# Optimization experiments

Hardware: AMD Instinct MI355X
Metric: run time of the kernel (lower is better)

The kernel has to match this reference:

```python
import jax, jax.numpy as jnp
import numpy as np

D_MODEL = 2048
DT_RANK = 64


def setup_inputs() -> dict:
    key = jax.random.key(0)
    ks = jax.random.split(key, 9)
    x = jax.random.normal(ks[0], (4, 2048, D_MODEL), dtype=jnp.float32)
    A = jax.random.normal(ks[1], (D_MODEL, D_MODEL), dtype=jnp.float32)
    B = jax.random.normal(ks[2], (D_MODEL, D_MODEL), dtype=jnp.float32)
    C = jax.random.normal(ks[3], (D_MODEL, D_MODEL), dtype=jnp.float32)
    Dp = jax.random.normal(ks[4], (1, D_MODEL), dtype=jnp.float32)
    # dt_project: Linear(d_model -> dt_rank); dt_project_out: Linear(dt_rank -> d_model)
    lim1 = 1.0 / np.sqrt(D_MODEL)
    W1 = jax.random.uniform(ks[5], (DT_RANK, D_MODEL), minval=-lim1, maxval=lim1, dtype=jnp.float32)
    b1 = jax.random.uniform(ks[6], (DT_RANK,), minval=-lim1, maxval=lim1, dtype=jnp.float32)
    lim2 = 1.0 / np.sqrt(DT_RANK)
    W2 = jax.random.uniform(ks[7], (D_MODEL, DT_RANK), minval=-lim2, maxval=lim2, dtype=jnp.float32)
    b2 = jax.random.uniform(ks[8], (D_MODEL,), minval=-lim2, maxval=lim2, dtype=jnp.float32)
    return {"x": x, "A": A, "B": B, "C": C, "Dp": Dp, "W1": W1, "b1": b1, "W2": W2, "b2": b2}


def reference(x, A, B, C, Dp, W1, b1, W2, b2):
    # dt = Linear_out(gelu(Linear_in(x)))  -- torch uses exact (erf) gelu
    h = jax.nn.gelu(jnp.einsum('bld,rd->blr', x, W1) + b1, approximate=False)
    dt = jnp.einsum('blr,dr->bld', h, W2) + b2
    # per-timestep loop collapses to one batched GEMM: x @ (A+B+C)
    out = jnp.einsum('bld,ds->bls', x, A + B + C)
    return out * dt + Dp  # Dp broadcasts (1, d_model)
```

## Files before the change

kernel.cpp:

```cpp
#include <hip/hip_runtime.h>
#include <stdint.h>

#define D 2048
#define R 64
#define M_TOTAL 8192

typedef float f32x4 __attribute__((ext_vector_type(4)));
typedef __bf16 bf16x8 __attribute__((ext_vector_type(8)));
typedef unsigned short u16x8 __attribute__((ext_vector_type(8)));
typedef unsigned short u16x4 __attribute__((ext_vector_type(4)));

__device__ __forceinline__ unsigned short f2bf(float f) {
  unsigned u = __builtin_bit_cast(unsigned, f);
  u += 0x7FFFu + ((u >> 16) & 1u);
  return (unsigned short)(u >> 16);
}

__device__ __forceinline__ void gload_lds16(const void* g, void* l) {
  __builtin_amdgcn_global_load_lds(
      (const __attribute__((address_space(1))) void*)g,
      (__attribute__((address_space(3))) void*)l, 16, 0, 0);
}

__global__ __launch_bounds__(256) void prep_kernel(
    const float* __restrict__ x, const float* __restrict__ A,
    const float* __restrict__ B, const float* __restrict__ C,
    const float* __restrict__ w1, const float* __restrict__ b1,
    const float* __restrict__ w2,
    unsigned short* __restrict__ xbf, unsigned short* __restrict__ st,
    unsigned short* __restrict__ w2bf, unsigned short* __restrict__ hbf) {
  __shared__ unsigned short plds[10240];
  int t = threadIdx.x;
  int bx = blockIdx.x;
  if (bx < 128) {
    int m0 = bx * 64;
    int row = t >> 2, c8 = (t & 3) * 8;
    const float* xp = x + (size_t)(m0 + row) * D + c8;
    const float* wp = w1 + (size_t)row * D + c8;
    unsigned short* xop = xbf + (size_t)(m0 + row) * D + c8;
    unsigned short* sX = plds;
    unsigned short* sW = plds + 5120;
    int w = t >> 6, lm = t & 15, lk = (t & 63) >> 4;
    f32x4 acc[4] = {};
    float4 rx0 = *(const float4*)(xp);
    float4 rx1 = *(const float4*)(xp + 4);
    float4 rw0 = *(const float4*)(wp);
    float4 rw1 = *(const float4*)(wp + 4);
#pragma unroll 1
    for (int kt = 0; kt < 64; ++kt) {
      int buf = (kt & 1) * 2560;
      u16x8 ox = { f2bf(rx0.x), f2bf(rx0.y), f2bf(rx0.z), f2bf(rx0.w),
                   f2bf(rx1.x), f2bf(rx1.y), f2bf(rx1.z), f2bf(rx1.w) };
      u16x8 ow = { f2bf(rw0.x), f2bf(rw0.y), f2bf(rw0.z), f2bf(rw0.w),
                   f2bf(rw1.x), f2bf(rw1.y), f2bf(rw1.z), f2bf(rw1.w) };
      *(u16x8*)(sX + buf + row * 40 + c8) = ox;
      *(u16x8*)(sW + buf + row * 40 + c8) = ow;
      *(u16x8*)(xop + kt * 32) = ox;
      __syncthreads();
      if (kt < 63) {
        rx0 = *(const float4*)(xp + (kt + 1) * 32);
        rx1 = *(const float4*)(xp + (kt + 1) * 32 + 4);
        rw0 = *(const float4*)(wp + (kt + 1) * 32);
        rw1 = *(const float4*)(wp + (kt + 1) * 32 + 4);
      }
      bf16x8 a = __builtin_bit_cast(bf16x8, *(const u16x8*)(sX + buf + (w * 16 + lm) * 40 + lk * 8));
#pragma unroll
      for (int j = 0; j < 4; ++j) {
        bf16x8 b = __builtin_bit_cast(bf16x8, *(const u16x8*)(sW + buf + (j * 16 + lm) * 40 + lk * 8));
        acc[j] = __builtin_amdgcn_mfma_f32_16x16x32_bf16(a, b, acc[j], 0, 0, 0);
      }
    }
    int m_base = m0 + w * 16 + lk * 4;
#pragma unroll
    for (int j = 0; j < 4; ++j) {
      int n = j * 16 + lm;
      float bv = b1[n];
#pragma unroll
      for (int r = 0; r < 4; ++r) {
        float v = acc[j][r] + bv;
        float g = 0.5f * v * (1.0f + erff(v * 0.70710678118654752f));
        hbf[(size_t)(m_base + r) * R + n] = f2bf(g);
      }
    }
  } else if (bx < 1152) {
    unsigned short (*lds)[68] = (unsigned short(*)[68])plds;
    int id = bx - 128;
    int tk = id >> 5, tn = id & 31;
    int k0 = tk * 64, n0 = tn * 64;
#pragma unroll
    for (int q = 0; q < 4; ++q) {
      int row = q * 16 + (t >> 4);
      int col = (t & 15) * 4;
      size_t off = (size_t)(k0 + row) * D + n0 + col;
      float4 a = *(const float4*)(A + off);
      float4 b = *(const float4*)(B + off);
      float4 c = *(const float4*)(C + off);
      u16x4 o = { f2bf(a.x + b.x + c.x), f2bf(a.y + b.y + c.y),
                  f2bf(a.z + b.z + c.z), f2bf(a.w + b.w + c.w) };
      *(u16x4*)(&lds[row][col]) = o;
    }
    __syncthreads();
    int n = t >> 2, kc = (t & 3) * 16;
    u16x8 v0, v1;
#pragma unroll
    for (int jj = 0; jj < 8; ++jj) v0[jj] = lds[kc + jj][n];
#pragma unroll
    for (int jj = 0; jj < 8; ++jj) v1[jj] = lds[kc + 8 + jj][n];
    size_t ooff = (size_t)(n0 + n) * D + k0 + kc;
    *(u16x8*)(st + ooff) = v0;
    *(u16x8*)(st + ooff + 8) = v1;
  } else {
    const int NW4 = (D * R) / 4;
    for (int i = (bx - 1152) * 256 + t; i < NW4; i += 8 * 256) {
      float4 v = ((const float4*)w2)[i];
      u16x4 o = { f2bf(v.x), f2bf(v.y), f2bf(v.z), f2bf(v.w) };
      *(u16x4*)(w2bf + (size_t)i * 4) = o;
    }
  }
}

__global__ __launch_bounds__(512, 2) void gemm_kernel(
    const unsigned short* __restrict__ xbf, const unsigned short* __restrict__ st,
    const unsigned short* __restrict__ hbf, const unsigned short* __restrict__ w2bf,
    const float* __restrict__ b2, const float* __restrict__ dp,
    float* __restrict__ out) {
  __shared__ unsigned short sA[2 * 16384];
  __shared__ unsigned short sB[2 * 16384];
  const int tid = threadIdx.x;
  const int w = tid >> 6, l = tid & 63, lk = l >> 4, lm = l & 15;
  const int wm = w >> 2, wn = w & 3;
  int bid = blockIdx.x;
  int wg = (bid & 7) * 32 + (bid >> 3);
  int mb = wg >> 3, nb = wg & 7;
  int m0 = mb * 256, n0 = nb * 256;

  const int kg = (tid & 7) ^ ((tid >> 3) & 7);
  const unsigned short* gA = xbf + (size_t)(m0 + (tid >> 3)) * D + kg * 8;
  const unsigned short* gB = st + (size_t)(n0 + (tid >> 3)) * D + kg * 8;
  const int dstw = w * 512;

  const int s7 = lm & 7;
  const int gsw0 = (lk ^ s7) * 8;
  const int gsw1 = ((4 | lk) ^ s7) * 8;
  const int arow = (wm * 128 + lm) * 64;
  const int brow = (wn * 64 + lm) * 64;

  f32x4 acc[8][4] = {};

#define STAGE(gptr, sbuf, T, h) do { \
    const unsigned short* g_ = (gptr) + (size_t)((h) * 128) * D + (T) * 64; \
    unsigned short* d_ = (sbuf) + (((T) & 1) * 16384 + (h) * 8192 + dstw); \
    gload_lds16(g_, d_); \
    gload_lds16(g_ + 64 * D, d_ + 4096); } while (0)

#define LD8(buf, off) __builtin_bit_cast(bf16x8, *(const u16x8*)((buf) + (off)))

  STAGE(gA, sA, 0, 0); STAGE(gA, sA, 0, 1);
  STAGE(gB, sB, 0, 0); STAGE(gB, sB, 0, 1);
  asm volatile("s_waitcnt vmcnt(0)" ::: "memory");
  __builtin_amdgcn_s_barrier();

  const int NT = D / 64;
#pragma unroll 1
  for (int kt = 0; kt < NT; ++kt) {
    const unsigned short* bufA = sA + (kt & 1) * 16384;
    const unsigned short* bufB = sB + (kt & 1) * 16384;
    bf16x8 a[4][2], b0[2][2], b1[2][2];

    #pragma unroll
    for (int i = 0; i < 4; ++i) {
      a[i][0] = LD8(bufA, arow + i * 1024 + gsw0);
      a[i][1] = LD8(bufA, arow + i * 1024 + gsw1);
    }
    #pragma unroll
    for (int j = 0; j < 2; ++j) {
      b0[j][0] = LD8(bufB, brow + j * 1024 + gsw0);
      b0[j][1] = LD8(bufB, brow + j * 1024 + gsw1);
    }
    if (kt + 1 < NT) { STAGE(gA, sA, kt + 1, 0); STAGE(gA, sA, kt + 1, 1); }
    __builtin_amdgcn_s_barrier();
    asm volatile("s_waitcnt lgkmcnt(0)" ::: "memory");
    __builtin_amdgcn_s_setprio(1);
    #pragma unroll
    for (int i = 0; i < 4; ++i)
      #pragma unroll
      for (int j = 0; j < 2; ++j) {
        acc[i][j] = __builtin_amdgcn_mfma_f32_16x16x32_bf16(a[i][0], b0[j][0], acc[i][j], 0, 0, 0);
        acc[i][j] = __builtin_amdgcn_mfma_f32_16x16x32_bf16(a[i][1], b0[j][1], acc[i][j], 0, 0, 0);
      }
    __builtin_amdgcn_s_setprio(0);
    __builtin_amdgcn_s_barrier();

    #pragma unroll
    for (int j = 0; j < 2; ++j) {
      b1[j][0] = LD8(bufB, brow + (j + 2) * 1024 + gsw0);
      b1[j][1] = LD8(bufB, brow + (j + 2) * 1024 + gsw1);
    }
    if (kt + 1 < NT) STAGE(gB, sB, kt + 1, 0);
    __builtin_amdgcn_s_barrier();
    asm volatile("s_waitcnt lgkmcnt(0)" ::: "memory");
    __builtin_amdgcn_s_setprio(1);
    #pragma unroll
    for (int i = 0; i < 4; ++i)
      #pragma unroll
      for (int j = 0; j < 2; ++j) {
        acc[i][j + 2] = __builtin_amdgcn_mfma_f32_16x16x32_bf16(a[i][0], b1[j][0], acc[i][j + 2], 0, 0, 0);
        acc[i][j + 2] = __builtin_amdgcn_mfma_f32_16x16x32_bf16(a[i][1], b1[j][1], acc[i][j + 2], 0, 0, 0);
      }
    __builtin_amdgcn_s_setprio(0);
    __builtin_amdgcn_s_barrier();

    #pragma unroll
    for (int i = 0; i < 4; ++i) {
      a[i][0] = LD8(bufA, arow + (i + 4) * 1024 + gsw0);
      a[i][1] = LD8(bufA, arow + (i + 4) * 1024 + gsw1);
    }
    if (kt + 1 < NT) STAGE(gB, sB, kt + 1, 1);
    __builtin_amdgcn_s_barrier();
    asm volatile("s_waitcnt lgkmcnt(0)" ::: "memory");
    __builtin_amdgcn_s_setprio(1);
    #pragma unroll
    for (int i = 0; i < 4; ++i)
      #pragma unroll
      for (int j = 0; j < 2; ++j) {
        acc[i + 4][j + 2] = __builtin_amdgcn_mfma_f32_16x16x32_bf16(a[i][0], b1[j][0], acc[i + 4][j + 2], 0, 0, 0);
        acc[i + 4][j + 2] = __builtin_amdgcn_mfma_f32_16x16x32_bf16(a[i][1], b1[j][1], acc[i + 4][j + 2], 0, 0, 0);
      }
    __builtin_amdgcn_s_setprio(0);
    __builtin_amdgcn_s_barrier();

    __builtin_amdgcn_s_setprio(1);
    #pragma unroll
    for (int i = 0; i < 4; ++i)
      #pragma unroll
      for (int j = 0; j < 2; ++j) {
        acc[i + 4][j] = __builtin_amdgcn_mfma_f32_16x16x32_bf16(a[i][0], b0[j][0], acc[i + 4][j], 0, 0, 0);
        acc[i + 4][j] = __builtin_amdgcn_mfma_f32_16x16x32_bf16(a[i][1], b0[j][1], acc[i + 4][j], 0, 0, 0);
      }
    __builtin_amdgcn_s_setprio(0);
    asm volatile("s_waitcnt vmcnt(0)" ::: "memory");
    __builtin_amdgcn_s_barrier();
  }

  bf16x8 wb0[4], wb1[4];
  float b2v[4], dpv[4];
#pragma unroll
  for (int j = 0; j < 4; ++j) {
    int n = n0 + wn * 64 + j * 16 + lm;
    const u16x8* wp = (const u16x8*)(w2bf + (size_t)n * R + lk * 8);
    wb0[j] = __builtin_bit_cast(bf16x8, wp[0]);
    wb1[j] = __builtin_bit_cast(bf16x8, wp[4]);
    b2v[j] = b2[n];
    dpv[j] = dp[n];
  }
#pragma unroll
  for (int mi = 0; mi < 8; ++mi) {
    int hrow = m0 + wm * 128 + mi * 16 + lm;
    const u16x8* hp = (const u16x8*)(hbf + (size_t)hrow * R + lk * 8);
    bf16x8 ha0 = __builtin_bit_cast(bf16x8, hp[0]);
    bf16x8 ha1 = __builtin_bit_cast(bf16x8, hp[4]);
    int mbase = m0 + wm * 128 + mi * 16 + lk * 4;
#pragma unroll
    for (int j = 0; j < 4; ++j) {
      f32x4 dt = {};
      dt = __builtin_amdgcn_mfma_f32_16x16x32_bf16(ha0, wb0[j], dt, 0, 0, 0);
      dt = __builtin_amdgcn_mfma_f32_16x16x32_bf16(ha1, wb1[j], dt, 0, 0, 0);
      int n = n0 + wn * 64 + j * 16 + lm;
#pragma unroll
      for (int r = 0; r < 4; ++r) {
        float val = acc[mi][j][r] * (dt[r] + b2v[j]) + dpv[j];
        out[(size_t)(mbase + r) * D + n] = val;
      }
    }
  }
#undef STAGE
#undef LD8
}

extern "C" void kernel_launch(void* const* d_in, const int* in_sizes, int n_in,
                              void* d_out, int out_size, void* d_ws, size_t ws_size,
                              hipStream_t stream) {
  const float* x  = (const float*)d_in[0];
  const float* A  = (const float*)d_in[1];
  const float* B  = (const float*)d_in[2];
  const float* C  = (const float*)d_in[3];
  const float* Dp = (const float*)d_in[4];
  const float* W1 = (const float*)d_in[5];
  const float* b1 = (const float*)d_in[6];
  const float* W2 = (const float*)d_in[7];
  const float* b2 = (const float*)d_in[8];
  float* out = (float*)d_out;

  uint8_t* ws = (uint8_t*)d_ws;
  unsigned short* xbf  = (unsigned short*)ws;
  unsigned short* st   = (unsigned short*)(ws + (32u << 20));
  unsigned short* w2bf = (unsigned short*)(ws + (40u << 20));
  unsigned short* hbf  = (unsigned short*)(ws + (41u << 20));

  prep_kernel<<<1160, 256, 0, stream>>>(x, A, B, C, W1, b1, W2, xbf, st, w2bf, hbf);
  gemm_kernel<<<256, 512, 0, stream>>>(xbf, st, hbf, w2bf, b2, Dp, out);
}
```

Measured before the change: 119.0 us.

## Split prep kernel K dimension across 512-thread blocks with swizzled LDS and deeper prefetch

```diff
diff --git a/kernel.cpp b/kernel.cpp
--- a/kernel.cpp
+++ b/kernel.cpp
@@ -22,85 +22,110 @@
       (__attribute__((address_space(3))) void*)l, 16, 0, 0);
 }
 
-__global__ __launch_bounds__(256) void prep_kernel(
+__global__ __launch_bounds__(512) void prep_kernel(
     const float* __restrict__ x, const float* __restrict__ A,
     const float* __restrict__ B, const float* __restrict__ C,
     const float* __restrict__ w1, const float* __restrict__ b1,
     const float* __restrict__ w2,
     unsigned short* __restrict__ xbf, unsigned short* __restrict__ st,
     unsigned short* __restrict__ w2bf, unsigned short* __restrict__ hbf) {
-  __shared__ unsigned short plds[10240];
-  int t = threadIdx.x;
-  int bx = blockIdx.x;
+  __shared__ unsigned short plds[16384];
+  const int t = threadIdx.x;
+  const int bx = blockIdx.x;
+
   if (bx < 128) {
-    int m0 = bx * 64;
-    int row = t >> 2, c8 = (t & 3) * 8;
-    const float* xp = x + (size_t)(m0 + row) * D + c8;
-    const float* wp = w1 + (size_t)row * D + c8;
-    unsigned short* xop = xbf + (size_t)(m0 + row) * D + c8;
     unsigned short* sX = plds;
-    unsigned short* sW = plds + 5120;
-    int w = t >> 6, lm = t & 15, lk = (t & 63) >> 4;
+    unsigned short* sW = plds + 8192;
+    const int m0 = bx * 64;
+    const int kh = t >> 8;
+    const int row = (t & 255) >> 2;
+    const int c = t & 3;
+    const float* xp = x + (size_t)(m0 + row) * D + kh * 1024 + c * 8;
+    const float* wp = w1 + (size_t)row * D + kh * 1024 + c * 8;
+    unsigned short* xop = xbf + (size_t)(m0 + row) * D + kh * 1024 + c * 8;
+    const int wslot = (c ^ ((row >> 1) & 3)) * 8;
+    unsigned short* sXw = sX + kh * 4096 + row * 32 + wslot;
+    unsigned short* sWw = sW + kh * 4096 + row * 32 + wslot;
+    const int w = t >> 6, l = t & 63, lm = l & 15, lk = l >> 4;
+    const int khw = w >> 2, wg = w & 3;
+    const int rslot = (lk ^ ((lm >> 1) & 3)) * 8;
+    const unsigned short* sXr = sX + khw * 4096 + (wg * 16 + lm) * 32 + rslot;
+    const unsigned short* sWr = sW + khw * 4096 + lm * 32 + rslot;
+
     f32x4 acc[4] = {};
-    float4 rx0 = *(const float4*)(xp);
-    float4 rx1 = *(const float4*)(xp + 4);
-    float4 rw0 = *(const float4*)(wp);
-    float4 rw1 = *(const float4*)(wp + 4);
+    float4 rx[2][2], rw[2][2];
+    rx[0][0] = *(const float4*)(xp);      rx[0][1] = *(const float4*)(xp + 4);
+    rw[0][0] = *(const float4*)(wp);      rw[0][1] = *(const float4*)(wp + 4);
+    rx[1][0] = *(const float4*)(xp + 32); rx[1][1] = *(const float4*)(xp + 36);
+    rw[1][0] = *(const float4*)(wp + 32); rw[1][1] = *(const float4*)(wp + 36);
+
 #pragma unroll 1
-    for (int kt = 0; kt < 64; ++kt) {
-      int buf = (kt & 1) * 2560;
-      u16x8 ox = { f2bf(rx0.x), f2bf(rx0.y), f2bf(rx0.z), f2bf(rx0.w),
-                   f2bf(rx1.x), f2bf(rx1.y), f2bf(rx1.z), f2bf(rx1.w) };
-      u16x8 ow = { f2bf(rw0.x), f2bf(rw0.y), f2bf(rw0.z), f2bf(rw0.w),
-                   f2bf(rw1.x), f2bf(rw1.y), f2bf(rw1.z), f2bf(rw1.w) };
-      *(u16x8*)(sX + buf + row * 40 + c8) = ox;
-      *(u16x8*)(sW + buf + row * 40 + c8) = ow;
+    for (int kt = 0; kt < 32; ++kt) {
+      const int s = kt & 1;
+      const int buf = s * 2048;
+      u16x8 ox = { f2bf(rx[s][0].x), f2bf(rx[s][0].y), f2bf(rx[s][0].z), f2bf(rx[s][0].w),
+                   f2bf(rx[s][1].x), f2bf(rx[s][1].y), f2bf(rx[s][1].z), f2bf(rx[s][1].w) };
+      u16x8 ow = { f2bf(rw[s][0].x), f2bf(rw[s][0].y), f2bf(rw[s][0].z), f2bf(rw[s][0].w),
+                   f2bf(rw[s][1].x), f2bf(rw[s][1].y), f2bf(rw[s][1].z), f2bf(rw[s][1].w) };
+      *(u16x8*)(sXw + buf) = ox;
+      *(u16x8*)(sWw + buf) = ow;
       *(u16x8*)(xop + kt * 32) = ox;
+      if (kt + 2 < 32) {
+        rx[s][0] = *(const float4*)(xp + (kt + 2) * 32);
+        rx[s][1] = *(const float4*)(xp + (kt + 2) * 32 + 4);
+        rw[s][0] = *(const float4*)(wp + (kt + 2) * 32);
+        rw[s][1] = *(const float4*)(wp + (kt + 2) * 32 + 4);
+      }
       __syncthreads();
-      if (kt < 63) {
-        rx0 = *(const float4*)(xp + (kt + 1) * 32);
-        rx1 = *(const float4*)(xp + (kt + 1) * 32 + 4);
-        rw0 = *(const float4*)(wp + (kt + 1) * 32);
-        rw1 = *(const float4*)(wp + (kt + 1) * 32 + 4);
-      }
-      bf16x8 a = __builtin_bit_cast(bf16x8, *(const u16x8*)(sX + buf + (w * 16 + lm) * 40 + lk * 8));
+      bf16x8 a = __builtin_bit_cast(bf16x8, *(const u16x8*)(sXr + buf));
 #pragma unroll
       for (int j = 0; j < 4; ++j) {
-        bf16x8 b = __builtin_bit_cast(bf16x8, *(const u16x8*)(sW + buf + (j * 16 + lm) * 40 + lk * 8));
+        bf16x8 b = __builtin_bit_cast(bf16x8, *(const u16x8*)(sWr + buf + j * 512));
         acc[j] = __builtin_amdgcn_mfma_f32_16x16x32_bf16(a, b, acc[j], 0, 0, 0);
       }
     }
-    int m_base = m0 + w * 16 + lk * 4;
-#pragma unroll
-    for (int j = 0; j < 4; ++j) {
-      int n = j * 16 + lm;
-      float bv = b1[n];
-#pragma unroll
-      for (int r = 0; r < 4; ++r) {
-        float v = acc[j][r] + bv;
-        float g = 0.5f * v * (1.0f + erff(v * 0.70710678118654752f));
-        hbf[(size_t)(m_base + r) * R + n] = f2bf(g);
-      }
-    }
-  } else if (bx < 1152) {
+
+    __syncthreads();
+    float* red = (float*)plds;
+    if (khw == 1) {
+#pragma unroll
+      for (int j = 0; j < 4; ++j)
+        *(f32x4*)(red + (j * 256 + wg * 64 + l) * 4) = acc[j];
+    }
+    __syncthreads();
+    if (khw == 0) {
+      int m_base = m0 + wg * 16 + lk * 4;
+#pragma unroll
+      for (int j = 0; j < 4; ++j) {
+        f32x4 o = *(const f32x4*)(red + (j * 256 + wg * 64 + l) * 4);
+        int n = j * 16 + lm;
+        float bv = b1[n];
+#pragma unroll
+        for (int r = 0; r < 4; ++r) {
+          float v = acc[j][r] + o[r] + bv;
+          float g = 0.5f * v * (1.0f + erff(v * 0.70710678118654752f));
+          hbf[(size_t)(m_base + r) * R + n] = f2bf(g);
+        }
+      }
+    }
+  } else if (bx < 640) {
     unsigned short (*lds)[68] = (unsigned short(*)[68])plds;
-    int id = bx - 128;
-    int tk = id >> 5, tn = id & 31;
-    int k0 = tk * 64, n0 = tn * 64;
+    const int id = bx - 128;
+    const int k0 = (id >> 5) * 128, n0 = (id & 31) * 64;
 #pragma unroll
     for (int q = 0; q < 4; ++q) {
-      int row = q * 16 + (t >> 4);
+      int rowq = q * 32 + (t >> 4);
       int col = (t & 15) * 4;
-      size_t off = (size_t)(k0 + row) * D + n0 + col;
+      size_t off = (size_t)(k0 + rowq) * D + n0 + col;
       float4 a = *(const float4*)(A + off);
       float4 b = *(const float4*)(B + off);
-      float4 c = *(const float4*)(C + off);
-      u16x4 o = { f2bf(a.x + b.x + c.x), f2bf(a.y + b.y + c.y),
-                  f2bf(a.z + b.z + c.z), f2bf(a.w + b.w + c.w) };
-      *(u16x4*)(&lds[row][col]) = o;
+      float4 cc = *(const float4*)(C + off);
+      u16x4 o = { f2bf(a.x + b.x + cc.x), f2bf(a.y + b.y + cc.y),
+                  f2bf(a.z + b.z + cc.z), f2bf(a.w + b.w + cc.w) };
+      *(u16x4*)(&lds[rowq][col]) = o;
     }
     __syncthreads();
-    int n = t >> 2, kc = (t & 3) * 16;
+    const int n = t >> 3, kc = (t & 7) * 16;
     u16x8 v0, v1;
 #pragma unroll
     for (int jj = 0; jj < 8; ++jj) v0[jj] = lds[kc + jj][n];
@@ -111,7 +136,7 @@
     *(u16x8*)(st + ooff + 8) = v1;
   } else {
     const int NW4 = (D * R) / 4;
-    for (int i = (bx - 1152) * 256 + t; i < NW4; i += 8 * 256) {
+    for (int i = (bx - 640) * 512 + t; i < NW4; i += 4 * 512) {
       float4 v = ((const float4*)w2)[i];
       u16x4 o = { f2bf(v.x), f2bf(v.y), f2bf(v.z), f2bf(v.w) };
       *(u16x4*)(w2bf + (size_t)i * 4) = o;
@@ -297,6 +322,6 @@
   unsigned short* w2bf = (unsigned short*)(ws + (40u << 20));
   unsigned short* hbf  = (unsigned short*)(ws + (41u << 20));
 
-  prep_kernel<<<1160, 256, 0, stream>>>(x, A, B, C, W1, b1, W2, xbf, st, w2bf, hbf);
+  prep_kernel<<<644, 512, 0, stream>>>(x, A, B, C, W1, b1, W2, xbf, st, w2bf, hbf);
   gemm_kernel<<<256, 512, 0, stream>>>(xbf, st, hbf, w2bf, b2, Dp, out);
 }
```

New measurement: 157.0 us. +32.0%, slower.
